# Kernel optimization log

Measured on AMD Instinct MI355X. Metric: run time of the kernel, lower is better.

Reference implementation:

```python
import jax, jax.numpy as jnp
import numpy as np

B, V, F, NT, NR, R = 4096, 200, 4, 16, 5, 16
G = NT * NR  # 80
MAX_RHO = 12.0
NLIG = 7
EPS = 1e-5
TWO_PI = 2.0 * np.pi


def setup_inputs() -> dict:
    key = jax.random.key(0)
    ks = jax.random.split(key, 16)
    input_feat = jax.random.normal(ks[0], (B, V, F), dtype=jnp.float32)
    rho = jax.random.uniform(ks[1], (B, V, 1), dtype=jnp.float32) * MAX_RHO
    theta = jax.random.uniform(ks[2], (B, V, 1), dtype=jnp.float32) * TWO_PI
    mask = (jax.random.uniform(ks[3], (B, V, 1)) < 0.9).astype(jnp.float32)
    # gaussian centers on a polar grid (per input feature channel)
    rc = jnp.linspace(0.0, MAX_RHO, NR)
    tc = jnp.linspace(0.0, TWO_PI, NT, endpoint=False)
    mu_rho = jnp.broadcast_to(jnp.repeat(rc, NT), (F, G)) + 0.05 * jax.random.normal(ks[4], (F, G))
    mu_theta = jnp.broadcast_to(jnp.tile(tc, NR), (F, G)) + 0.05 * jax.random.normal(ks[5], (F, G))
    sigma_rho = jnp.full((F, G), MAX_RHO / 8.0, dtype=jnp.float32)
    sigma_theta = jnp.ones((F, G), dtype=jnp.float32)
    conv_W = jax.random.normal(ks[6], (F, G, G), dtype=jnp.float32) / np.sqrt(G)
    conv_b = jnp.zeros((F, G), dtype=jnp.float32)
    fc1_W = jax.random.normal(ks[7], (G, F * G), dtype=jnp.float32) / np.sqrt(F * G)
    fc1_b = jnp.zeros((G,), dtype=jnp.float32)
    fc2_W = jax.random.normal(ks[8], (64, G * G), dtype=jnp.float32) / np.sqrt(G * G)
    fc2_b = jnp.zeros((64,), dtype=jnp.float32)
    fco_W = jax.random.normal(ks[9], (NLIG, 64), dtype=jnp.float32) / 8.0
    fco_b = jnp.zeros((NLIG,), dtype=jnp.float32)
    return dict(input_feat=input_feat, rho=rho, theta=theta, mask=mask,
                mu_rho=mu_rho, mu_theta=mu_theta, sigma_rho=sigma_rho, sigma_theta=sigma_theta,
                conv_W=conv_W, conv_b=conv_b, fc1_W=fc1_W, fc1_b=fc1_b,
                fc2_W=fc2_W, fc2_b=fc2_b, fco_W=fco_W, fco_b=fco_b)


def reference(input_feat, rho, theta, mask, mu_rho, mu_theta, sigma_rho, sigma_theta,
              conv_W, conv_b, fc1_W, fc1_b, fc2_W, fc2_b, fco_W, fco_b):
    rot = (TWO_PI / R) * jnp.arange(R, dtype=jnp.float32)

    def conv_feat(x_f, mr, mt, sr, st, W, b):
        # x_f: [B,V,1]; mr/mt/sr/st: [G]; W: [G,G]; b: [G]
        @jax.checkpoint
        def step(carry, ang):
            th = jnp.mod(theta + ang, TWO_PI)                      # [B,V,1]
            g = jnp.exp(-(rho - mr) ** 2 / (sr ** 2 + EPS)
                        - (th - mt) ** 2 / (st ** 2 + EPS)) * mask  # [B,V,G]
            agg = jnp.einsum('bvg,bvo->bg', g, x_f)                 # [B,G]
            return carry, jax.nn.relu(agg @ W + b)
        _, outs = jax.lax.scan(step, None, rot)                      # [R,B,G]
        return outs.max(axis=0)                                      # [B,G]

    descs = [conv_feat(input_feat[:, :, i:i + 1], mu_rho[i], mu_theta[i],
                       sigma_rho[i], sigma_theta[i], conv_W[i], conv_b[i])
             for i in range(F)]
    x = jnp.stack(descs, axis=1).reshape(input_feat.shape[0], -1)   # [B, F*G]
    x = jax.nn.relu(x @ fc1_W.T + fc1_b)                             # [B, G]
    gram = (x.T @ x / x.shape[0]).reshape(1, -1)                     # [1, G*G]
    # dropout is identity at inference
    h = jax.nn.relu(gram @ fc2_W.T + fc2_b)                          # [1, 64]
    return h @ fco_W.T + fco_b                                       # [1, NLIG]
```

## Files before the change

### kernel.cpp

```cpp
#include <hip/hip_runtime.h>
#include <hip/hip_bf16.h>

#define BB 4096
#define VV 200
#define FF 4
#define GG 80
#define RR 16
#define NLIG 7
#define PVMAX 216
#define TWO_PI_F 6.2831853071795864769f
#define ANG_STEP 0.39269908169872414f
#define INV_ANG_STEP 2.5464790894703255f
#define LOG2E_F 1.4426950408889634f

typedef float v2f __attribute__((ext_vector_type(2)));

__device__ __forceinline__ float fexp2(float x) {
#if __has_builtin(__builtin_amdgcn_exp2f)
    return __builtin_amdgcn_exp2f(x);
#else
    return exp2f(x);
#endif
}

__device__ __forceinline__ v2f pk_fma(v2f a, v2f b, v2f c) {
    v2f d;
    asm("v_pk_fma_f32 %0, %1, %2, %3" : "=v"(d) : "v"(a), "v"(b), "v"(c));
    return d;
}
__device__ __forceinline__ v2f pk_mul(v2f a, v2f b) {
    v2f d;
    asm("v_pk_mul_f32 %0, %1, %2" : "=v"(d) : "v"(a), "v"(b));
    return d;
}

template<int C>
__device__ __forceinline__ void chain(const v2f (&Kp)[8], v2f (&aggE)[8],
                                      v2f (&aggO)[8], float M, float B) {
    const float B2 = B * B;
    v2f u;  u.x = M;  u.y = M * B;
    v2f w2; w2.x = B2; w2.y = B2;
    #pragma unroll
    for (int i = 0; i < 8; ++i) {
        const int idx = ((2 * i + 16 - C) & 15) >> 1;
        if constexpr ((C & 1) == 0) aggE[idx] = pk_fma(u, Kp[i], aggE[idx]);
        else                        aggO[idx] = pk_fma(u, Kp[i], aggO[idx]);
        if (i < 7) u = pk_mul(u, w2);
    }
}

__global__ __launch_bounds__(320, 6) void masif_main(
    const float* __restrict__ xin,
    const float* __restrict__ rho,
    const float* __restrict__ theta,
    const float* __restrict__ mask,
    const float* __restrict__ mu_rho,
    const float* __restrict__ mu_theta,
    const float* __restrict__ sigma_rho,
    const float* __restrict__ sigma_theta,
    const float* __restrict__ conv_W,
    const float* __restrict__ conv_b,
    const float* __restrict__ fc1_W,
    const float* __restrict__ fc1_b,
    float* __restrict__ xbuf)
{
    const int b = blockIdx.x;
    const int t = threadIdx.x;
    const int f = t / GG;
    const int g = t % GG;
    const int lane = t & 63;
    const int w = t >> 6;

    __shared__ __align__(16) char uni[PVMAX * 8 + FF * PVMAX * 4];
    float2* pv_ra = reinterpret_cast<float2*>(uni);
    float (*pv_x)[PVMAX] = reinterpret_cast<float(*)[PVMAX]>(uni + PVMAX * 8);
    float* desc_s = reinterpret_cast<float*>(uni);
    float* hp_s   = reinterpret_cast<float*>(uni + 1280);

    __shared__ int cntw[5][RR];
    __shared__ int ps[RR + 1];
    __shared__ float aggL[FF][RR][GG];

    float rh = 0.f, a0 = 0.f, mx0 = 0.f, mx1 = 0.f, mx2 = 0.f, mx3 = 0.f;
    int j0 = 0;
    bool keep = false;
    if (t < VV) {
        const int idx = b * VV + t;
        const float th = theta[idx];
        const float m  = mask[idx];
        keep = (m != 0.0f);
        rh = rho[idx];
        j0 = (int)(th * INV_ANG_STEP);
        if (j0 > RR - 1) j0 = RR - 1;
        a0 = fmaf(-(float)j0, ANG_STEP, th);
        const float4 xv = *reinterpret_cast<const float4*>(&xin[idx * 4]);
        mx0 = m * xv.x; mx1 = m * xv.y; mx2 = m * xv.z; mx3 = m * xv.w;
    }

    const float mr  = mu_rho[f * GG + g];
    const float mt  = mu_theta[f * GG + g];
    const float sr  = sigma_rho[f * GG + g];
    const float st  = sigma_theta[f * GG + g];
    const float nisr2 = -LOG2E_F / (sr * sr + 1e-5f);
    const float nist2 = -LOG2E_F / (st * st + 1e-5f);
    const float c1 = 2.0f * ANG_STEP * nist2;
    v2f Kp[8];
    #pragma unroll
    for (int i = 0; i < 8; ++i) {
        const float m0 = (float)(2 * i), m1 = (float)(2 * i + 1);
        Kp[i].x = fexp2(nist2 * (ANG_STEP * ANG_STEP) * m0 * m0);
        Kp[i].y = fexp2(nist2 * (ANG_STEP * ANG_STEP) * m1 * m1);
    }

    int rank = 0, cnt_lane = 0;
    #pragma unroll
    for (int c = 0; c < RR; ++c) {
        const unsigned long long mbl = __ballot(keep && (j0 == c));
        if (keep && (j0 == c))
            rank = (int)__popcll(mbl & ((1ull << lane) - 1ull));
        if (lane == c) cnt_lane = (int)__popcll(mbl);
    }
    if (lane < RR) cntw[w][lane] = cnt_lane;
    __syncthreads();

    if (t == 0) {
        int s = 0;
        #pragma unroll
        for (int c = 0; c < RR; ++c) {
            ps[c] = s;
            const int cc = cntw[0][c] + cntw[1][c] + cntw[2][c]
                         + cntw[3][c] + cntw[4][c];
            s += (cc + 1) & ~1;
        }
        ps[RR] = s;
    }
    if (t < PVMAX) {
        pv_ra[t] = make_float2(0.f, 0.f);
        pv_x[0][t] = 0.f; pv_x[1][t] = 0.f; pv_x[2][t] = 0.f; pv_x[3][t] = 0.f;
    }
    __syncthreads();

    if (keep) {
        int off = 0;
        #pragma unroll
        for (int w2 = 0; w2 < 4; ++w2)
            if (w2 < w) off += cntw[w2][j0];
        const int pos = ps[j0] + off + rank;
        pv_ra[pos] = make_float2(rh, a0);
        pv_x[0][pos] = mx0; pv_x[1][pos] = mx1;
        pv_x[2][pos] = mx2; pv_x[3][pos] = mx3;
    }
    __syncthreads();

    v2f aggE[8], aggO[8];
    #pragma unroll
    for (int i = 0; i < 8; ++i) {
        aggE[i].x = 0.f; aggE[i].y = 0.f;
        aggO[i].x = 0.f; aggO[i].y = 0.f;
    }

    int sprev = 0;
#define CLS(C) { \
        const int send = __builtin_amdgcn_readfirstlane(ps[(C) + 1]); \
        for (int v = sprev; v < send; v += 2) { \
            const float4 ra2 = *reinterpret_cast<const float4*>(&pv_ra[v]); \
            const v2f s2 = *reinterpret_cast<const v2f*>(&pv_x[f][v]); \
            const float drA = ra2.x - mr, xA = ra2.y - mt; \
            const float arA = (drA * drA) * nisr2; \
            const float MA = fexp2(fmaf(xA * xA, nist2, arA)) * s2.x; \
            const float BA = fexp2(xA * c1); \
            const float drB = ra2.z - mr, xB = ra2.w - mt; \
            const float arB = (drB * drB) * nisr2; \
            const float MB = fexp2(fmaf(xB * xB, nist2, arB)) * s2.y; \
            const float BBv = fexp2(xB * c1); \
            chain<(C)>(Kp, aggE, aggO, MA, BA); \
            chain<(C)>(Kp, aggE, aggO, MB, BBv); \
        } \
        sprev = send; }
    CLS(0)  CLS(1)  CLS(2)  CLS(3)
    CLS(4)  CLS(5)  CLS(6)  CLS(7)
    CLS(8)  CLS(9)  CLS(10) CLS(11)
    CLS(12) CLS(13) CLS(14) CLS(15)
#undef CLS

    #pragma unroll
    for (int k = 0; k < 8; ++k) {
        aggL[f][2 * k][g]     = aggE[k].x + aggO[(k + 7) & 7].y;
        aggL[f][2 * k + 1][g] = aggE[k].y + aggO[k].x;
    }
    __syncthreads();

    v2f racc2[RR];
    {
        const float cb = conv_b[f * GG + g];
        #pragma unroll
        for (int r = 0; r < RR; ++r) { racc2[r].x = cb; racc2[r].y = 0.f; }
    }
    for (int g4 = 0; g4 < GG; g4 += 4) {
        const float* wp = &conv_W[(f * GG + g4) * GG + g];
        v2f wA, wB;
        wA.x = wp[0];      wA.y = wp[GG];
        wB.x = wp[2 * GG]; wB.y = wp[3 * GG];
        #pragma unroll
        for (int r = 0; r < RR; ++r) {
            const float4 a4 = *reinterpret_cast<const float4*>(&aggL[f][r][g4]);
            v2f aA, aB;
            aA.x = a4.x; aA.y = a4.y;
            aB.x = a4.z; aB.y = a4.w;
            racc2[r] = pk_fma(aA, wA, racc2[r]);
            racc2[r] = pk_fma(aB, wB, racc2[r]);
        }
    }
    float mxr = racc2[0].x + racc2[0].y;
    #pragma unroll
    for (int r = 1; r < RR; ++r) mxr = fmaxf(mxr, racc2[r].x + racc2[r].y);
    desc_s[f * GG + g] = fmaxf(mxr, 0.0f);

    __syncthreads();

    {
        const v2f* wrow = reinterpret_cast<const v2f*>(&fc1_W[g * (FF * GG) + f * GG]);
        const v2f* drow = reinterpret_cast<const v2f*>(&desc_s[f * GG]);
        v2f a2; a2.x = 0.f; a2.y = 0.f;
        #pragma unroll 4
        for (int k = 0; k < GG / 2; ++k) a2 = pk_fma(drow[k], wrow[k], a2);
        hp_s[f * GG + g] = a2.x + a2.y;
    }
    __syncthreads();
    if (t < GG) {
        const float a1 = ((hp_s[t] + hp_s[GG + t]) + (hp_s[2 * GG + t] + hp_s[3 * GG + t]))
                         + fc1_b[t];
        xbuf[b * GG + t] = fmaxf(a1, 0.0f);
    }
}

__global__ __launch_bounds__(256) void gram_partial(
    const float* __restrict__ xbuf,
    float* __restrict__ gpart)
{
    const int blk = blockIdx.x;
    const int t = threadIdx.x;
    __shared__ float xs[64][GG];

    for (int i = t; i < 64 * GG; i += 256) {
        int bb = i / GG, jj = i % GG;
        xs[bb][jj] = xbuf[(blk * 64 + bb) * GG + jj];
    }
    __syncthreads();

    const int ti = t / 16, tj = t % 16;
    float acc[5][5];
    #pragma unroll
    for (int u = 0; u < 5; ++u)
        #pragma unroll
        for (int w = 0; w < 5; ++w) acc[u][w] = 0.0f;

    for (int bb = 0; bb < 64; ++bb) {
        float xi[5], xj[5];
        #pragma unroll
        for (int u = 0; u < 5; ++u) { xi[u] = xs[bb][ti * 5 + u]; xj[u] = xs[bb][tj * 5 + u]; }
        #pragma unroll
        for (int u = 0; u < 5; ++u)
            #pragma unroll
            for (int w = 0; w < 5; ++w)
                acc[u][w] = fmaf(xi[u], xj[w], acc[u][w]);
    }

    #pragma unroll
    for (int u = 0; u < 5; ++u)
        #pragma unroll
        for (int w = 0; w < 5; ++w)
            gpart[blk * (GG * GG) + (ti * 5 + u) * GG + (tj * 5 + w)] = acc[u][w];
}

__global__ __launch_bounds__(128) void head_partial(
    const float* __restrict__ gpart,
    const float* __restrict__ fc2_W,
    float* __restrict__ hpp)
{
    const int p = blockIdx.x;
    const int t = threadIdx.x;
    __shared__ float gs[100];

    if (t < 100) {
        const int k = p * 100 + t;
        float s = 0.f;
        #pragma unroll 8
        for (int q = 0; q < 64; ++q) s += gpart[q * (GG * GG) + k];
        gs[t] = s * (1.0f / 4096.0f);
    }
    __syncthreads();
    if (t < 64) {
        const float* w = &fc2_W[t * (GG * GG) + p * 100];
        float a = 0.f;
        #pragma unroll 4
        for (int k = 0; k < 100; ++k) a = fmaf(gs[k], w[k], a);
        hpp[p * 64 + t] = a;
    }
}

__global__ __launch_bounds__(256) void head_final(
    const float* __restrict__ hpp,
    const float* __restrict__ fc2_b,
    const float* __restrict__ fco_W,
    const float* __restrict__ fco_b,
    float* __restrict__ out)
{
    const int t = threadIdx.x;
    const int part = t >> 6, j = t & 63;
    __shared__ float hq[4][64];
    __shared__ float hs[64];
    float a = 0.f;
    #pragma unroll 4
    for (int p = part * 16; p < part * 16 + 16; ++p) a += hpp[p * 64 + j];
    hq[part][j] = a;
    __syncthreads();
    if (t < 64)
        hs[t] = fmaxf(((hq[0][t] + hq[1][t]) + (hq[2][t] + hq[3][t])) + fc2_b[t], 0.0f);
    __syncthreads();
    if (t < NLIG) {
        float o = fco_b[t];
        #pragma unroll
        for (int jj = 0; jj < 64; ++jj) o = fmaf(hs[jj], fco_W[t * 64 + jj], o);
        out[t] = o;
    }
}

extern "C" void kernel_launch(void* const* d_in, const int* in_sizes, int n_in,
                              void* d_out, int out_size, void* d_ws, size_t ws_size,
                              hipStream_t stream) {
    const float* input_feat  = (const float*)d_in[0];
    const float* rho         = (const float*)d_in[1];
    const float* theta       = (const float*)d_in[2];
    const float* mask        = (const float*)d_in[3];
    const float* mu_rho      = (const float*)d_in[4];
    const float* mu_theta    = (const float*)d_in[5];
    const float* sigma_rho   = (const float*)d_in[6];
    const float* sigma_theta = (const float*)d_in[7];
    const float* conv_W      = (const float*)d_in[8];
    const float* conv_b      = (const float*)d_in[9];
    const float* fc1_W       = (const float*)d_in[10];
    const float* fc1_b       = (const float*)d_in[11];
    const float* fc2_W       = (const float*)d_in[12];
    const float* fc2_b       = (const float*)d_in[13];
    const float* fco_W       = (const float*)d_in[14];
    const float* fco_b       = (const float*)d_in[15];

    float* xbuf  = (float*)d_ws;
    float* gpart = (float*)((char*)d_ws + (size_t)BB * GG * 4);
    float* hpp   = (float*)((char*)d_ws + (size_t)BB * GG * 4
                                        + (size_t)64 * GG * GG * 4);

    masif_main<<<BB, 320, 0, stream>>>(input_feat, rho, theta, mask,
                                       mu_rho, mu_theta, sigma_rho, sigma_theta,
                                       conv_W, conv_b, fc1_W, fc1_b, xbuf);
    gram_partial<<<64, 256, 0, stream>>>(xbuf, gpart);
    head_partial<<<64, 128, 0, stream>>>(gpart, fc2_W, hpp);
    head_final<<<1, 256, 0, stream>>>(hpp, fc2_b, fco_W, fco_b, (float*)d_out);
}
```

Before: 317.3 us.

## Precompute per-vertex Gaussian terms when sigmas are uniform across block

```diff
diff --git a/kernel.cpp b/kernel.cpp
--- a/kernel.cpp
+++ b/kernel.cpp
@@ -48,6 +48,17 @@
         if (i < 7) u = pk_mul(u, w2);
     }
 }
+
+#define OFF_PV_RA 0
+#define OFF_PV_VB 1728
+#define OFF_PV_X  3456
+#define OFF_CNTW  6912
+#define OFF_PS    7232
+#define OFF_SSIG  7300
+#define OFF_AGGL  0
+#define OFF_DESC  20480
+#define OFF_HP    21760
+#define UNI_SIZE  23104
 
 __global__ __launch_bounds__(320, 6) void masif_main(
     const float* __restrict__ xin,
@@ -71,15 +82,24 @@
     const int lane = t & 63;
     const int w = t >> 6;
 
-    __shared__ __align__(16) char uni[PVMAX * 8 + FF * PVMAX * 4];
-    float2* pv_ra = reinterpret_cast<float2*>(uni);
-    float (*pv_x)[PVMAX] = reinterpret_cast<float(*)[PVMAX]>(uni + PVMAX * 8);
-    float* desc_s = reinterpret_cast<float*>(uni);
-    float* hp_s   = reinterpret_cast<float*>(uni + 1280);
-
-    __shared__ int cntw[5][RR];
-    __shared__ int ps[RR + 1];
-    __shared__ float aggL[FF][RR][GG];
+    __shared__ __align__(16) char U[UNI_SIZE];
+    float2* pv_ra = reinterpret_cast<float2*>(U + OFF_PV_RA);
+    float2* pv_vb = reinterpret_cast<float2*>(U + OFF_PV_VB);
+    float (*pv_x)[PVMAX] = reinterpret_cast<float(*)[PVMAX]>(U + OFF_PV_X);
+    int (*cntw)[RR] = reinterpret_cast<int(*)[RR]>(U + OFF_CNTW);
+    int* ps = reinterpret_cast<int*>(U + OFF_PS);
+    float* ssig = reinterpret_cast<float*>(U + OFF_SSIG);
+    float (*aggL)[RR][GG] = reinterpret_cast<float(*)[RR][GG]>(U + OFF_AGGL);
+    float* desc_s = reinterpret_cast<float*>(U + OFF_DESC);
+    float* hp_s = reinterpret_cast<float*>(U + OFF_HP);
+
+    const float mr  = mu_rho[f * GG + g];
+    const float mt  = mu_theta[f * GG + g];
+    const float sr  = sigma_rho[f * GG + g];
+    const float st  = sigma_theta[f * GG + g];
+    const float nisr2 = -LOG2E_F / (sr * sr + 1e-5f);
+    const float nist2 = -LOG2E_F / (st * st + 1e-5f);
+    const float c1 = 2.0f * ANG_STEP * nist2;
 
     float rh = 0.f, a0 = 0.f, mx0 = 0.f, mx1 = 0.f, mx2 = 0.f, mx3 = 0.f;
     int j0 = 0;
@@ -96,14 +116,8 @@
         const float4 xv = *reinterpret_cast<const float4*>(&xin[idx * 4]);
         mx0 = m * xv.x; mx1 = m * xv.y; mx2 = m * xv.z; mx3 = m * xv.w;
     }
-
-    const float mr  = mu_rho[f * GG + g];
-    const float mt  = mu_theta[f * GG + g];
-    const float sr  = sigma_rho[f * GG + g];
-    const float st  = sigma_theta[f * GG + g];
-    const float nisr2 = -LOG2E_F / (sr * sr + 1e-5f);
-    const float nist2 = -LOG2E_F / (st * st + 1e-5f);
-    const float c1 = 2.0f * ANG_STEP * nist2;
+    if (t == 0) { ssig[0] = nisr2; ssig[1] = nist2; }
+
     v2f Kp[8];
     #pragma unroll
     for (int i = 0; i < 8; ++i) {
@@ -123,6 +137,15 @@
     if (lane < RR) cntw[w][lane] = cnt_lane;
     __syncthreads();
 
+    const float s_nisr2 = ssig[0], s_nist2 = ssig[1];
+    const int myflag = (__float_as_int(nisr2) == __float_as_int(s_nisr2)) &&
+                       (__float_as_int(nist2) == __float_as_int(s_nist2));
+    float va = 0.f, Bv = 0.f;
+    if (t < VV) {
+        const float s_c1 = 2.0f * ANG_STEP * s_nist2;
+        va = fmaf(a0 * a0, s_nist2, (rh * rh) * s_nisr2);
+        Bv = fexp2(s_c1 * a0);
+    }
     if (t == 0) {
         int s = 0;
         #pragma unroll
@@ -136,9 +159,10 @@
     }
     if (t < PVMAX) {
         pv_ra[t] = make_float2(0.f, 0.f);
+        pv_vb[t] = make_float2(0.f, 0.f);
         pv_x[0][t] = 0.f; pv_x[1][t] = 0.f; pv_x[2][t] = 0.f; pv_x[3][t] = 0.f;
     }
-    __syncthreads();
+    const int uniOK = __syncthreads_and(myflag);
 
     if (keep) {
         int off = 0;
@@ -147,6 +171,7 @@
             if (w2 < w) off += cntw[w2][j0];
         const int pos = ps[j0] + off + rank;
         pv_ra[pos] = make_float2(rh, a0);
+        pv_vb[pos] = make_float2(va, Bv);
         pv_x[0][pos] = mx0; pv_x[1][pos] = mx1;
         pv_x[2][pos] = mx2; pv_x[3][pos] = mx3;
     }
@@ -159,8 +184,36 @@
         aggO[i].x = 0.f; aggO[i].y = 0.f;
     }
 
-    int sprev = 0;
-#define CLS(C) { \
+    if (uniOK) {
+        const float ct1 = -2.0f * nist2 * mt;
+        const float ct2 = -2.0f * nisr2 * mr;
+        const float Cc  = fmaf(mt * mt, nist2, (mr * mr) * nisr2);
+        const float Bt  = fexp2(-c1 * mt);
+        int sprev = 0;
+#define CLSF(C) { \
+        const int send = __builtin_amdgcn_readfirstlane(ps[(C) + 1]); \
+        for (int v = sprev; v < send; v += 2) { \
+            const float4 ra2 = *reinterpret_cast<const float4*>(&pv_ra[v]); \
+            const float4 vb2 = *reinterpret_cast<const float4*>(&pv_vb[v]); \
+            const v2f s2 = *reinterpret_cast<const v2f*>(&pv_x[f][v]); \
+            const float tA = fmaf(ra2.y, ct1, fmaf(ra2.x, ct2, vb2.x + Cc)); \
+            const float MsA = fexp2(tA) * s2.x; \
+            const float BA = vb2.y * Bt; \
+            const float tB = fmaf(ra2.w, ct1, fmaf(ra2.z, ct2, vb2.z + Cc)); \
+            const float MsB = fexp2(tB) * s2.y; \
+            const float BBv = vb2.w * Bt; \
+            chain<(C)>(Kp, aggE, aggO, MsA, BA); \
+            chain<(C)>(Kp, aggE, aggO, MsB, BBv); \
+        } \
+        sprev = send; }
+        CLSF(0)  CLSF(1)  CLSF(2)  CLSF(3)
+        CLSF(4)  CLSF(5)  CLSF(6)  CLSF(7)
+        CLSF(8)  CLSF(9)  CLSF(10) CLSF(11)
+        CLSF(12) CLSF(13) CLSF(14) CLSF(15)
+#undef CLSF
+    } else {
+        int sprev = 0;
+#define CLSS(C) { \
         const int send = __builtin_amdgcn_readfirstlane(ps[(C) + 1]); \
         for (int v = sprev; v < send; v += 2) { \
             const float4 ra2 = *reinterpret_cast<const float4*>(&pv_ra[v]); \
@@ -177,11 +230,13 @@
             chain<(C)>(Kp, aggE, aggO, MB, BBv); \
         } \
         sprev = send; }
-    CLS(0)  CLS(1)  CLS(2)  CLS(3)
-    CLS(4)  CLS(5)  CLS(6)  CLS(7)
-    CLS(8)  CLS(9)  CLS(10) CLS(11)
-    CLS(12) CLS(13) CLS(14) CLS(15)
-#undef CLS
+        CLSS(0)  CLSS(1)  CLSS(2)  CLSS(3)
+        CLSS(4)  CLSS(5)  CLSS(6)  CLSS(7)
+        CLSS(8)  CLSS(9)  CLSS(10) CLSS(11)
+        CLSS(12) CLSS(13) CLSS(14) CLSS(15)
+#undef CLSS
+    }
+    __syncthreads();
 
     #pragma unroll
     for (int k = 0; k < 8; ++k) {
```

After: 322.2 us. Within noise of the previous version (+1.6%).
